# Kernel tuning notes

Hardware: AMD Instinct MI355X
Metric: run time of the kernel (lower is better)

Reference implementation:

```python
import jax, jax.numpy as jnp
import numpy as np

N, C, H, W = 2, 256, 64, 64   # feature map
K = 64                        # number of boxes
PH = PW = 7                   # output_size
SCALE = 0.25                  # spatial_scale
SR = 2                        # sampling_ratio


def setup_inputs() -> dict:
    key = jax.random.key(0)
    k1, k2, k3, k4 = jax.random.split(key, 4)
    features = jax.random.normal(k1, (N, C, H, W), dtype=jnp.float32)
    masks = jax.random.uniform(k2, (K, C, H, W), dtype=jnp.float32)
    bidx = jax.random.randint(k3, (K,), 0, N).astype(jnp.float32)
    # box corners in image coordinates [0, W/SCALE)
    pts = jax.random.uniform(k4, (K, 4), minval=0.0, maxval=W / SCALE, dtype=jnp.float32)
    x1 = jnp.minimum(pts[:, 0], pts[:, 2]); x2 = jnp.maximum(pts[:, 0], pts[:, 2])
    y1 = jnp.minimum(pts[:, 1], pts[:, 3]); y2 = jnp.maximum(pts[:, 1], pts[:, 3])
    boxes = jnp.stack([bidx, x1, y1, x2, y2], axis=1)  # [K, 5]
    return {"features": features, "boxes": boxes, "masks": masks}


def _bilinear(fmap, ys, xs):
    """Bilinear sample fmap[C,H,W] at all (ys x xs) grid points -> [C, Ny, Nx].
    Matches torchvision RoIAlign edge handling (zero outside [-1, L])."""
    Hh, Ww = fmap.shape[1], fmap.shape[2]

    def ax(v, L):
        valid = (v >= -1.0) & (v <= L)
        vc = jnp.clip(v, 0.0, L - 1.0)
        lo = jnp.floor(vc).astype(jnp.int32)
        hi = jnp.minimum(lo + 1, L - 1)
        fr = vc - lo.astype(vc.dtype)
        return valid, lo, hi, fr

    vy, yl, yh, ly = ax(ys, Hh)
    vx, xl, xh, lx = ax(xs, Ww)
    hy, hx = 1.0 - ly, 1.0 - lx
    g = lambda yi, xi: fmap[:, yi[:, None], xi[None, :]]  # [C, Ny, Nx]
    val = (hy[:, None] * hx[None, :]) * g(yl, xl) \
        + (hy[:, None] * lx[None, :]) * g(yl, xh) \
        + (ly[:, None] * hx[None, :]) * g(yh, xl) \
        + (ly[:, None] * lx[None, :]) * g(yh, xh)
    return val * (vy[:, None] & vx[None, :]).astype(val.dtype)


def reference(features, boxes, masks):
    b = boxes[:, 0].astype(jnp.int32)                      # batch index per box
    coords = jax.lax.stop_gradient(boxes[:, 1:]) * SCALE   # roi_align has no box grad
    off = (jnp.arange(SR, dtype=jnp.float32) + 0.5) / SR   # sub-bin offsets

    def one(bi, box, mask):
        fmap = features[bi] * mask                         # masked clone [C,H,W]
        x1, y1, x2, y2 = box
        roi_w = jnp.maximum(x2 - x1, 1.0)
        roi_h = jnp.maximum(y2 - y1, 1.0)
        bin_h, bin_w = roi_h / PH, roi_w / PW
        ys = (y1 + (jnp.arange(PH, dtype=jnp.float32)[:, None] + off) * bin_h).reshape(-1)
        xs = (x1 + (jnp.arange(PW, dtype=jnp.float32)[:, None] + off) * bin_w).reshape(-1)
        vals = _bilinear(fmap, ys, xs)                     # [C, PH*SR, PW*SR]
        return vals.reshape(fmap.shape[0], PH, SR, PW, SR).mean(axis=(2, 4))

    return jax.vmap(one)(b, coords, masks)                 # [K, C, PH, PW]
```

## Files before the change

kernel.cpp:

```cpp
#include <hip/hip_runtime.h>
#include <hip/hip_bf16.h>


constexpr int N_ = 2, C_ = 256, H_ = 64, W_ = 64;
constexpr int K_ = 64, PH_ = 7, PW_ = 7, SR_ = 2;
constexpr float SCALE_ = 0.25f;

__global__ __launch_bounds__(256)
void masked_roialign_kernel(const float* __restrict__ features,
                            const float* __restrict__ boxes,
                            const float* __restrict__ masks,
                            float* __restrict__ out) {
    const int k  = blockIdx.x;
    const int cg = blockIdx.y;
    const int t  = threadIdx.x;
    const int c   = cg * 4 + (t >> 6);
    const int bin = t & 63;
    if (bin >= PH_ * PW_) return;
    const int ph = bin / PW_;
    const int pw = bin - ph * PW_;

    const float* bx = boxes + k * 5;
    const int   b  = (int)bx[0];
    const float x1 = bx[1] * SCALE_;
    const float y1 = bx[2] * SCALE_;
    const float x2 = bx[3] * SCALE_;
    const float y2 = bx[4] * SCALE_;
    const float roi_w = fmaxf(x2 - x1, 1.0f);
    const float roi_h = fmaxf(y2 - y1, 1.0f);
    const float bin_w = roi_w * (1.0f / PW_);
    const float bin_h = roi_h * (1.0f / PH_);

    const float* __restrict__ f = features + ((size_t)b * C_ + c) * (H_ * W_);
    const float* __restrict__ m = masks    + ((size_t)k * C_ + c) * (H_ * W_);

    float acc = 0.0f;
#pragma unroll
    for (int iy = 0; iy < SR_; ++iy) {
        const float y  = y1 + ((float)ph + ((float)iy + 0.5f) * 0.5f) * bin_h;
        const bool  vy = (y >= -1.0f) && (y <= (float)H_);
        const float yc = fminf(fmaxf(y, 0.0f), (float)(H_ - 1));
        const int   yl = (int)yc;
        const int   yh = min(yl + 1, H_ - 1);
        const float ly = yc - (float)yl;
        const float hy = 1.0f - ly;
#pragma unroll
        for (int ix = 0; ix < SR_; ++ix) {
            const float x  = x1 + ((float)pw + ((float)ix + 0.5f) * 0.5f) * bin_w;
            const bool  vx = (x >= -1.0f) && (x <= (float)W_);
            const float xc = fminf(fmaxf(x, 0.0f), (float)(W_ - 1));
            const int   xl = (int)xc;
            const int   xh = min(xl + 1, W_ - 1);
            const float lx = xc - (float)xl;
            const float hx = 1.0f - lx;

            const int i00 = yl * W_ + xl, i01 = yl * W_ + xh;
            const int i10 = yh * W_ + xl, i11 = yh * W_ + xh;
            const float v00 = f[i00] * m[i00];
            const float v01 = f[i01] * m[i01];
            const float v10 = f[i10] * m[i10];
            const float v11 = f[i11] * m[i11];
            float val = hy * hx * v00 + hy * lx * v01
                      + ly * hx * v10 + ly * lx * v11;
            acc += (vy && vx) ? val : 0.0f;
        }
    }
    out[(((size_t)k * C_ + c) * PH_ + ph) * PW_ + pw] = acc * 0.25f;
}

extern "C" void kernel_launch(void* const* d_in, const int* in_sizes, int n_in,
                              void* d_out, int out_size, void* d_ws, size_t ws_size,
                              hipStream_t stream) {
    const float* features = (const float*)d_in[0];
    const float* boxes    = (const float*)d_in[1];
    const float* masks    = (const float*)d_in[2];
    float* out            = (float*)d_out;

    dim3 grid(K_, C_ / 4);
    dim3 block(256);
    masked_roialign_kernel<<<grid, block, 0, stream>>>(features, boxes, masks, out);
}
```

Measured before the change: 339.8 us.

## Stage masked feature rows in LDS with coalesced float4 loads before bilinear sampling

Each block now loads the rows of features and masks covered by the box's vertical extent with coalesced float4 loads, multiplies them, and stores the masked product in shared memory. Bilinear sampling then reads from LDS instead of issuing scattered global loads to both tensors. Block size drops to 128 threads covering 2 channels instead of 4. The staging reads the full row width even though the box covers only part of it, so global traffic may grow in exchange for better coalescing, and it adds a barrier.

```diff
diff --git a/kernel.cpp b/kernel.cpp
--- a/kernel.cpp
+++ b/kernel.cpp
@@ -5,20 +5,19 @@
 constexpr int N_ = 2, C_ = 256, H_ = 64, W_ = 64;
 constexpr int K_ = 64, PH_ = 7, PW_ = 7, SR_ = 2;
 constexpr float SCALE_ = 0.25f;
+constexpr int CG = 2;
+constexpr int BT = 128;
 
-__global__ __launch_bounds__(256)
-void masked_roialign_kernel(const float* __restrict__ features,
-                            const float* __restrict__ boxes,
-                            const float* __restrict__ masks,
-                            float* __restrict__ out) {
+__global__ __launch_bounds__(BT)
+void masked_roialign_lds(const float* __restrict__ features,
+                         const float* __restrict__ boxes,
+                         const float* __restrict__ masks,
+                         float* __restrict__ out) {
+    __shared__ float prod[CG * H_ * W_];
+
     const int k  = blockIdx.x;
     const int cg = blockIdx.y;
     const int t  = threadIdx.x;
-    const int c   = cg * 4 + (t >> 6);
-    const int bin = t & 63;
-    if (bin >= PH_ * PW_) return;
-    const int ph = bin / PW_;
-    const int pw = bin - ph * PW_;
 
     const float* bx = boxes + k * 5;
     const int   b  = (int)bx[0];
@@ -31,8 +30,36 @@
     const float bin_w = roi_w * (1.0f / PW_);
     const float bin_h = roi_h * (1.0f / PH_);
 
-    const float* __restrict__ f = features + ((size_t)b * C_ + c) * (H_ * W_);
-    const float* __restrict__ m = masks    + ((size_t)k * C_ + c) * (H_ * W_);
+    const float ymin_c = fminf(fmaxf(y1 + 0.25f * bin_h, 0.0f), (float)(H_ - 1));
+    const float ymax_c = fminf(fmaxf(y1 + 6.75f * bin_h, 0.0f), (float)(H_ - 1));
+    const int ylo   = (int)ymin_c;
+    const int yhi   = min((int)ymax_c + 1, H_ - 1);
+    const int nrows = yhi - ylo + 1;
+
+#pragma unroll
+    for (int cl = 0; cl < CG; ++cl) {
+        const int c = cg * CG + cl;
+        const float4* __restrict__ f4 =
+            (const float4*)(features + ((size_t)b * C_ + c) * (H_ * W_) + ylo * W_);
+        const float4* __restrict__ m4 =
+            (const float4*)(masks    + ((size_t)k * C_ + c) * (H_ * W_) + ylo * W_);
+        float4* p4 = (float4*)(prod + cl * (H_ * W_));
+        const int nvec = nrows * (W_ / 4);
+        for (int i = t; i < nvec; i += BT) {
+            const float4 fv = f4[i];
+            const float4 mv = m4[i];
+            p4[i] = make_float4(fv.x * mv.x, fv.y * mv.y, fv.z * mv.z, fv.w * mv.w);
+        }
+    }
+    __syncthreads();
+
+    const int cl  = t >> 6;
+    const int bin = t & 63;
+    if (bin >= PH_ * PW_) return;
+    const int ph = bin / PW_;
+    const int pw = bin - ph * PW_;
+
+    const float* __restrict__ p = prod + cl * (H_ * W_);
 
     float acc = 0.0f;
 #pragma unroll
@@ -44,6 +71,8 @@
         const int   yh = min(yl + 1, H_ - 1);
         const float ly = yc - (float)yl;
         const float hy = 1.0f - ly;
+        const int   rl = yl - ylo;
+        const int   rh = yh - ylo;
 #pragma unroll
         for (int ix = 0; ix < SR_; ++ix) {
             const float x  = x1 + ((float)pw + ((float)ix + 0.5f) * 0.5f) * bin_w;
@@ -54,17 +83,16 @@
             const float lx = xc - (float)xl;
             const float hx = 1.0f - lx;
 
-            const int i00 = yl * W_ + xl, i01 = yl * W_ + xh;
-            const int i10 = yh * W_ + xl, i11 = yh * W_ + xh;
-            const float v00 = f[i00] * m[i00];
-            const float v01 = f[i01] * m[i01];
-            const float v10 = f[i10] * m[i10];
-            const float v11 = f[i11] * m[i11];
-            float val = hy * hx * v00 + hy * lx * v01
-                      + ly * hx * v10 + ly * lx * v11;
+            const float v00 = p[rl * W_ + xl];
+            const float v01 = p[rl * W_ + xh];
+            const float v10 = p[rh * W_ + xl];
+            const float v11 = p[rh * W_ + xh];
+            const float val = hy * hx * v00 + hy * lx * v01
+                            + ly * hx * v10 + ly * lx * v11;
             acc += (vy && vx) ? val : 0.0f;
         }
     }
+    const int c = cg * CG + cl;
     out[(((size_t)k * C_ + c) * PH_ + ph) * PW_ + pw] = acc * 0.25f;
 }
 
@@ -76,7 +104,7 @@
     const float* masks    = (const float*)d_in[2];
     float* out            = (float*)d_out;
 
-    dim3 grid(K_, C_ / 4);
-    dim3 block(256);
-    masked_roialign_kernel<<<grid, block, 0, stream>>>(features, boxes, masks, out);
+    dim3 grid(K_, C_ / CG);
+    dim3 block(BT);
+    masked_roialign_lds<<<grid, block, 0, stream>>>(features, boxes, masks, out);
 }
```

Result: no change. 342.5 us (+0.8%).
